# Optimization experiments

Hardware: AMD Instinct MI355X
Metric: run time of the kernel (lower is better)

## Reference

```python
import jax, jax.numpy as jnp
import numpy as np

N = 65536
E = 1048576
DIN = 64
DOUT = 64


def setup_inputs() -> dict:
    key = jax.random.key(0)
    ks = jax.random.split(key, 16)
    inp = {
        'feat': jax.random.normal(ks[0], (N, DIN), dtype=jnp.float32),
        'norm': jax.random.uniform(ks[1], (N, 1), dtype=jnp.float32),
        'src': jax.random.randint(ks[2], (E,), 0, N, dtype=jnp.int32),
        'dst': jax.random.randint(ks[3], (E,), 0, N, dtype=jnp.int32),
    }
    s = 0.05
    inp['W_self'] = jax.random.normal(ks[4], (DOUT, DIN)) * s
    inp['b_self'] = jnp.zeros((DOUT,), jnp.float32)
    inp['W_self_high'] = jax.random.normal(ks[5], (DOUT, DIN)) * s
    inp['b_self_high'] = jnp.zeros((DOUT,), jnp.float32)
    inp['W_neigh'] = jax.random.normal(ks[6], (DOUT, DIN)) * s
    inp['b_neigh'] = jnp.zeros((DOUT,), jnp.float32)
    inp['W_neigh_high'] = jax.random.normal(ks[7], (DOUT, DIN)) * s
    inp['b_neigh_high'] = jnp.zeros((DOUT,), jnp.float32)
    inp['W_id'] = jax.random.normal(ks[8], (DOUT, DIN)) * s
    inp['b_id'] = jnp.zeros((DOUT,), jnp.float32)
    inp['w_att_low'] = jax.random.normal(ks[9], (1, DOUT)) * s
    inp['w_att_high'] = jax.random.normal(ks[10], (1, DOUT)) * s
    inp['w_att_mlp'] = jax.random.normal(ks[11], (1, DOUT)) * s
    inp['W_att'] = jax.random.normal(ks[12], (3, 3)) * s
    return inp


def _linear(x, W, b):
    return x @ W.T + b


def _mean_agg(h, norm, src, dst, n_nodes):
    # copy_src('h','m') of (h * norm), then mean-reduce by dst node
    msg = (h * norm)[src]                                   # [E, D] gather
    summed = jax.ops.segment_sum(msg, dst, num_segments=n_nodes)
    deg = jax.ops.segment_sum(jnp.ones((dst.shape[0],), h.dtype), dst,
                              num_segments=n_nodes)
    return summed / jnp.maximum(deg, 1.0)[:, None]          # zero-in-degree -> 0


def reference(feat, norm, src, dst,
              W_self, b_self, W_self_high, b_self_high,
              W_neigh, b_neigh, W_neigh_high, b_neigh_high,
              W_id, b_id, w_att_low, w_att_high, w_att_mlp, W_att):
    n = feat.shape[0]
    # variant=True branch of acmgraphsage
    self_low = jax.nn.relu(_linear(feat, W_self, b_self))
    self_high = jax.nn.relu(_linear(feat, W_self_high, b_self_high))
    neigh_low = _mean_agg(jax.nn.relu(_linear(feat, W_neigh, b_neigh)),
                          norm, src, dst, n)
    neigh_high = _mean_agg(jax.nn.relu(_linear(feat, W_neigh_high, b_neigh_high)),
                           norm, src, dst, n)
    low = self_low + neigh_low
    high = self_high - neigh_high
    identity = jax.nn.relu(_linear(feat, W_id, b_id))
    # attention: sigmoid of per-branch scalar logits -> 3x3 mix -> softmax/T
    logits = jnp.concatenate([low @ w_att_low.T,
                              high @ w_att_high.T,
                              identity @ w_att_mlp.T], axis=1)   # [N, 3]
    att = jax.nn.softmax((jax.nn.sigmoid(logits) @ W_att.T) / 3.0, axis=1)
    rst = 3.0 * (att[:, 0:1] * low + att[:, 1:2] * high + att[:, 2:3] * identity)
    return rst
```

## Files before the change

### kernel.cpp

```cpp
#include <hip/hip_runtime.h>
#include <stdint.h>


#define NBLK 256
#define NBUC 1024
#define NPB  64
#define GCAP 2048
#define MTOT (NBUC * NBLK)

__device__ __forceinline__ void load_feat(const float* __restrict__ feat, size_t base,
                                          float* __restrict__ f) {
    const float4* fp = (const float4*)(feat + base);
#pragma unroll
    for (int i = 0; i < 16; ++i) {
        float4 v = fp[i];
        f[4 * i + 0] = v.x; f[4 * i + 1] = v.y;
        f[4 * i + 2] = v.z; f[4 * i + 3] = v.w;
    }
}

__device__ __forceinline__ uint32_t bf16_rne(float x) {
    uint32_t u = __float_as_uint(x);
    return (u + 0x7fffu + ((u >> 16) & 1u)) >> 16;
}

__global__ void __launch_bounds__(512)
k_tf_hist(const float* __restrict__ feat, const float* __restrict__ norm,
          const float* __restrict__ Wn, const float* __restrict__ bn,
          const float* __restrict__ Wnh, const float* __restrict__ bnh,
          uint32_t* __restrict__ h_pk,
          const int* __restrict__ dst, int* __restrict__ blk_cnt,
          int N, int E, int nTf)
{
    __shared__ int cnt[NBUC];
    int t = threadIdx.x;

    if ((int)blockIdx.x >= nTf) {
        int hb = blockIdx.x - nTf;
        for (int i = t; i < NBUC; i += 512) cnt[i] = 0;
        __syncthreads();
        int epb = (E + NBLK - 1) / NBLK;
        int eb = hb * epb;
        for (int i0 = t * 8; i0 < epb; i0 += 512 * 8) {
            int e = eb + i0;
            if (e + 8 <= E) {
                int4 d0 = *(const int4*)(dst + e);
                int4 d1 = *(const int4*)(dst + e + 4);
                atomicAdd(&cnt[((unsigned)d0.x) >> 6], 1);
                atomicAdd(&cnt[((unsigned)d0.y) >> 6], 1);
                atomicAdd(&cnt[((unsigned)d0.z) >> 6], 1);
                atomicAdd(&cnt[((unsigned)d0.w) >> 6], 1);
                atomicAdd(&cnt[((unsigned)d1.x) >> 6], 1);
                atomicAdd(&cnt[((unsigned)d1.y) >> 6], 1);
                atomicAdd(&cnt[((unsigned)d1.z) >> 6], 1);
                atomicAdd(&cnt[((unsigned)d1.w) >> 6], 1);
            } else {
                for (int j = 0; j < 8; ++j) {
                    int ee = e + j;
                    if (ee < E) atomicAdd(&cnt[((unsigned)dst[ee]) >> 6], 1);
                }
            }
        }
        __syncthreads();
        for (int i = t; i < NBUC; i += 512)
            blk_cnt[i * NBLK + hb] = cnt[i];
        return;
    }

    int nsub = t & 63;
    int q = __builtin_amdgcn_readfirstlane(t >> 6);
    int n = blockIdx.x * 64 + nsub;
    if (n >= N) return;

    size_t base = (size_t)n << 6;
    float f[64];
    load_feat(feat, base, f);
    float nr = norm[n];

    uint32_t pk[8];
#pragma unroll
    for (int jj = 0; jj < 8; ++jj) {
        int j = q * 8 + jj;
        const float4* rL = (const float4*)(Wn  + ((size_t)j << 6));
        const float4* rH = (const float4*)(Wnh + ((size_t)j << 6));
        float sL = 0.f, sH = 0.f;
#pragma unroll
        for (int k4 = 0; k4 < 16; ++k4) {
            float4 wL = rL[k4];
            float4 wH = rH[k4];
            sL = fmaf(f[4*k4+0], wL.x, sL); sL = fmaf(f[4*k4+1], wL.y, sL);
            sL = fmaf(f[4*k4+2], wL.z, sL); sL = fmaf(f[4*k4+3], wL.w, sL);
            sH = fmaf(f[4*k4+0], wH.x, sH); sH = fmaf(f[4*k4+1], wH.y, sH);
            sH = fmaf(f[4*k4+2], wH.z, sH); sH = fmaf(f[4*k4+3], wH.w, sH);
        }
        float oL = fmaxf(sL + bn[j],  0.f) * nr;
        float oH = fmaxf(sH + bnh[j], 0.f) * nr;
        pk[jj] = bf16_rne(oL) | (bf16_rne(oH) << 16);
    }
    uint4* pp = (uint4*)(h_pk + base + q * 8);
    pp[0] = make_uint4(pk[0], pk[1], pk[2], pk[3]);
    pp[1] = make_uint4(pk[4], pk[5], pk[6], pk[7]);
}

__global__ void __launch_bounds__(256)
k_scan_part(const int* __restrict__ cnt_in, int* __restrict__ part)
{
    __shared__ int red[256];
    int t = threadIdx.x;
    const int4* A4 = (const int4*)cnt_in;
    int4 v = A4[blockIdx.x * 256 + t];
    int s = v.x + v.y + v.z + v.w;
    red[t] = s;
    __syncthreads();
    for (int off = 128; off > 0; off >>= 1) {
        if (t < off) red[t] += red[t + off];
        __syncthreads();
    }
    if (t == 0) part[blockIdx.x] = red[0];
}

__global__ void __launch_bounds__(256)
k_scan_top(const int* __restrict__ part, int* __restrict__ top)
{
    __shared__ int s[256];
    int t = threadIdx.x;
    int mine = part[t];
    s[t] = mine;
    __syncthreads();
    for (int off = 1; off < 256; off <<= 1) {
        int v = s[t];
        int a = (t >= off) ? s[t - off] : 0;
        __syncthreads();
        s[t] = v + a;
        __syncthreads();
    }
    top[t] = s[t] - mine;
}

__global__ void __launch_bounds__(256)
k_scan_down(const int* __restrict__ cnt_in, const int* __restrict__ top,
            int* __restrict__ off_out)
{
    __shared__ int s[256];
    int t = threadIdx.x;
    const int4* A4 = (const int4*)cnt_in;
    int4 v = A4[blockIdx.x * 256 + t];
    int sum = v.x + v.y + v.z + v.w;
    s[t] = sum;
    __syncthreads();
    for (int off = 1; off < 256; off <<= 1) {
        int vv = s[t];
        int a = (t >= off) ? s[t - off] : 0;
        __syncthreads();
        s[t] = vv + a;
        __syncthreads();
    }
    int run = top[blockIdx.x] + s[t] - sum;
    int4 o;
    o.x = run; run += v.x;
    o.y = run; run += v.y;
    o.z = run; run += v.z;
    o.w = run; run += v.w;
    ((int4*)off_out)[blockIdx.x * 256 + t] = o;
    if (blockIdx.x == 255 && t == 255) off_out[MTOT] = run;
}

__global__ void __launch_bounds__(512)
k_bin_scatter(const int* __restrict__ src, const int* __restrict__ dst,
              const int* __restrict__ blk_off, uint32_t* __restrict__ ebuf, int E)
{
    __shared__ int base_[NBUC];
    __shared__ int cnt[NBUC];
    int t = threadIdx.x;
    for (int i = t; i < NBUC; i += 512) {
        base_[i] = blk_off[i * NBLK + blockIdx.x];
        cnt[i] = 0;
    }
    __syncthreads();
    int epb = (E + NBLK - 1) / NBLK;
    int eb = blockIdx.x * epb;
    for (int i0 = t * 8; i0 < epb; i0 += 512 * 8) {
        int e = eb + i0;
        if (e + 8 <= E) {
            int4 d0 = *(const int4*)(dst + e);
            int4 d1 = *(const int4*)(dst + e + 4);
            int4 s0 = *(const int4*)(src + e);
            int4 s1 = *(const int4*)(src + e + 4);
            int da[8] = { d0.x, d0.y, d0.z, d0.w, d1.x, d1.y, d1.z, d1.w };
            int sa[8] = { s0.x, s0.y, s0.z, s0.w, s1.x, s1.y, s1.z, s1.w };
#pragma unroll
            for (int j = 0; j < 8; ++j) {
                int b = ((unsigned)da[j]) >> 6;
                int r = atomicAdd(&cnt[b], 1);
                ebuf[base_[b] + r] = ((uint32_t)(da[j] & 63) << 16) | (uint32_t)sa[j];
            }
        } else {
            for (int j = 0; j < 8; ++j) {
                int ee = e + j;
                if (ee < E) {
                    int d = dst[ee];
                    int b = ((unsigned)d) >> 6;
                    int r = atomicAdd(&cnt[b], 1);
                    ebuf[base_[b] + r] = ((uint32_t)(d & 63) << 16) | (uint32_t)src[ee];
                }
            }
        }
    }
}

__global__ void __launch_bounds__(512)
k_gf(const uint32_t* __restrict__ h_pk, const int* __restrict__ blk_off,
     const uint32_t* __restrict__ ebuf,
     const float* __restrict__ feat,
     const float* __restrict__ Ws, const float* __restrict__ bs,
     const float* __restrict__ Wsh, const float* __restrict__ bsh,
     const float* __restrict__ Wid, const float* __restrict__ bid,
     const float* __restrict__ wl, const float* __restrict__ wh,
     const float* __restrict__ wm, const float* __restrict__ Watt,
     float* __restrict__ out, int N)
{
    __shared__ unsigned short sorted[GCAP];
    __shared__ int s_cnt[NPB];
    __shared__ int s_off[NPB];
    __shared__ uint32_t s_m[NPB][65];
    __shared__ float red[3][8][64];

    int b = blockIdx.x;
    int t = threadIdx.x;
    int es = blk_off[b * NBLK];
    int ee = blk_off[(b + 1) * NBLK];
    int ne = ee - es;
    if (ne > GCAP) ne = GCAP;
    if (t < NPB) s_cnt[t] = 0;
    __syncthreads();

    int ed[4], er[4], esrc[4];
#pragma unroll
    for (int i = 0; i < 4; ++i) {
        int idx = i * 512 + t;
        ed[i] = -1;
        if (idx < ne) {
            uint32_t v = ebuf[es + idx];
            ed[i] = (int)(v >> 16);
            esrc[i] = (int)(v & 0xffffu);
            er[i] = atomicAdd(&s_cnt[ed[i]], 1);
        }
    }
    __syncthreads();
    if (t < 64) {
        int c = s_cnt[t];
        int sc = c;
        for (int o = 1; o < 64; o <<= 1) {
            int u = __shfl_up(sc, o, 64);
            if (t >= o) sc += u;
        }
        s_off[t] = sc - c;
    }
    __syncthreads();
#pragma unroll
    for (int i = 0; i < 4; ++i)
        if (ed[i] >= 0) sorted[s_off[ed[i]] + er[i]] = (unsigned short)esrc[i];
    __syncthreads();

    int w = t >> 6, lane = t & 63;
    for (int dd = 0; dd < 8; ++dd) {
        int d = w * 8 + dd;
        int cd = s_cnt[d];
        int od = s_off[d];
        float accL = 0.f, accH = 0.f;
        int i = 0;
        for (; i + 8 <= cd; i += 8) {
            int s0 = sorted[od + i + 0];
            int s1 = sorted[od + i + 1];
            int s2 = sorted[od + i + 2];
            int s3 = sorted[od + i + 3];
            int s4 = sorted[od + i + 4];
            int s5 = sorted[od + i + 5];
            int s6 = sorted[od + i + 6];
            int s7 = sorted[od + i + 7];
            uint32_t v0 = h_pk[((size_t)s0 << 6) + lane];
            uint32_t v1 = h_pk[((size_t)s1 << 6) + lane];
            uint32_t v2 = h_pk[((size_t)s2 << 6) + lane];
            uint32_t v3 = h_pk[((size_t)s3 << 6) + lane];
            uint32_t v4 = h_pk[((size_t)s4 << 6) + lane];
            uint32_t v5 = h_pk[((size_t)s5 << 6) + lane];
            uint32_t v6 = h_pk[((size_t)s6 << 6) + lane];
            uint32_t v7 = h_pk[((size_t)s7 << 6) + lane];
            accL += (__uint_as_float(v0 << 16) + __uint_as_float(v1 << 16))
                  + (__uint_as_float(v2 << 16) + __uint_as_float(v3 << 16))
                  + (__uint_as_float(v4 << 16) + __uint_as_float(v5 << 16))
                  + (__uint_as_float(v6 << 16) + __uint_as_float(v7 << 16));
            accH += (__uint_as_float(v0 & 0xffff0000u) + __uint_as_float(v1 & 0xffff0000u))
                  + (__uint_as_float(v2 & 0xffff0000u) + __uint_as_float(v3 & 0xffff0000u))
                  + (__uint_as_float(v4 & 0xffff0000u) + __uint_as_float(v5 & 0xffff0000u))
                  + (__uint_as_float(v6 & 0xffff0000u) + __uint_as_float(v7 & 0xffff0000u));
        }
        for (; i + 4 <= cd; i += 4) {
            int s0 = sorted[od + i + 0];
            int s1 = sorted[od + i + 1];
            int s2 = sorted[od + i + 2];
            int s3 = sorted[od + i + 3];
            uint32_t v0 = h_pk[((size_t)s0 << 6) + lane];
            uint32_t v1 = h_pk[((size_t)s1 << 6) + lane];
            uint32_t v2 = h_pk[((size_t)s2 << 6) + lane];
            uint32_t v3 = h_pk[((size_t)s3 << 6) + lane];
            accL += (__uint_as_float(v0 << 16) + __uint_as_float(v1 << 16))
                  + (__uint_as_float(v2 << 16) + __uint_as_float(v3 << 16));
            accH += (__uint_as_float(v0 & 0xffff0000u) + __uint_as_float(v1 & 0xffff0000u))
                  + (__uint_as_float(v2 & 0xffff0000u) + __uint_as_float(v3 & 0xffff0000u));
        }
        for (; i < cd; ++i) {
            int s0 = sorted[od + i];
            uint32_t v0 = h_pk[((size_t)s0 << 6) + lane];
            accL += __uint_as_float(v0 << 16);
            accH += __uint_as_float(v0 & 0xffff0000u);
        }
        float inv = 1.f / fmaxf((float)cd, 1.f);
        s_m[d][lane] = bf16_rne(accL * inv) | (bf16_rne(accH * inv) << 16);
    }
    __syncthreads();

    int nsub = t & 63;
    int q = __builtin_amdgcn_readfirstlane(t >> 6);
    int n = b * 64 + nsub;
    size_t base = (size_t)n << 6;

    float f[64];
    load_feat(feat, base, f);

    float aL[8], aH[8], aI[8];
    float dLp = 0.f, dHp = 0.f, dIp = 0.f;
#pragma unroll
    for (int jj = 0; jj < 8; ++jj) {
        int j = q * 8 + jj;
        const float4* rL = (const float4*)(Ws  + ((size_t)j << 6));
        const float4* rH = (const float4*)(Wsh + ((size_t)j << 6));
        const float4* rI = (const float4*)(Wid + ((size_t)j << 6));
        float sL = 0.f, sH = 0.f, sI = 0.f;
#pragma unroll
        for (int k4 = 0; k4 < 16; ++k4) {
            float4 wL = rL[k4];
            float4 wH = rH[k4];
            float4 wI = rI[k4];
            sL = fmaf(f[4*k4+0], wL.x, sL); sL = fmaf(f[4*k4+1], wL.y, sL);
            sL = fmaf(f[4*k4+2], wL.z, sL); sL = fmaf(f[4*k4+3], wL.w, sL);
            sH = fmaf(f[4*k4+0], wH.x, sH); sH = fmaf(f[4*k4+1], wH.y, sH);
            sH = fmaf(f[4*k4+2], wH.z, sH); sH = fmaf(f[4*k4+3], wH.w, sH);
            sI = fmaf(f[4*k4+0], wI.x, sI); sI = fmaf(f[4*k4+1], wI.y, sI);
            sI = fmaf(f[4*k4+2], wI.z, sI); sI = fmaf(f[4*k4+3], wI.w, sI);
        }
        uint32_t mv = s_m[nsub][j];
        float lowj  = fmaxf(sL + bs[j],  0.f) + __uint_as_float(mv << 16);
        float highj = fmaxf(sH + bsh[j], 0.f) - __uint_as_float(mv & 0xffff0000u);
        float idj   = fmaxf(sI + bid[j], 0.f);
        aL[jj] = lowj; aH[jj] = highj; aI[jj] = idj;
        dLp = fmaf(lowj,  wl[j], dLp);
        dHp = fmaf(highj, wh[j], dHp);
        dIp = fmaf(idj,   wm[j], dIp);
    }

    red[0][q][nsub] = dLp;
    red[1][q][nsub] = dHp;
    red[2][q][nsub] = dIp;
    __syncthreads();
    float dL = 0.f, dH = 0.f, dI = 0.f;
#pragma unroll
    for (int p = 0; p < 8; ++p) {
        dL += red[0][p][nsub];
        dH += red[1][p][nsub];
        dI += red[2][p][nsub];
    }

    float s0 = 1.f / (1.f + expf(-dL));
    float s1 = 1.f / (1.f + expf(-dH));
    float s2 = 1.f / (1.f + expf(-dI));
    const float third = (1.f / 3.f);
    float z0 = (Watt[0] * s0 + Watt[1] * s1 + Watt[2] * s2) * third;
    float z1 = (Watt[3] * s0 + Watt[4] * s1 + Watt[5] * s2) * third;
    float z2 = (Watt[6] * s0 + Watt[7] * s1 + Watt[8] * s2) * third;
    float m = fmaxf(z0, fmaxf(z1, z2));
    float e0 = expf(z0 - m), e1 = expf(z1 - m), e2 = expf(z2 - m);
    float r = 3.f / (e0 + e1 + e2);
    float a0 = e0 * r, a1 = e1 * r, a2 = e2 * r;

    float o[8];
#pragma unroll
    for (int jj = 0; jj < 8; ++jj)
        o[jj] = a0 * aL[jj] + a1 * aH[jj] + a2 * aI[jj];
    float* po = out + base + q * 8;
    *(float4*)(po + 0) = make_float4(o[0], o[1], o[2], o[3]);
    *(float4*)(po + 4) = make_float4(o[4], o[5], o[6], o[7]);
}

extern "C" void kernel_launch(void* const* d_in, const int* in_sizes, int n_in,
                              void* d_out, int out_size, void* d_ws, size_t ws_size,
                              hipStream_t stream) {
    const float* feat         = (const float*)d_in[0];
    const float* norm         = (const float*)d_in[1];
    const int*   src          = (const int*)d_in[2];
    const int*   dst          = (const int*)d_in[3];
    const float* W_self       = (const float*)d_in[4];
    const float* b_self       = (const float*)d_in[5];
    const float* W_self_high  = (const float*)d_in[6];
    const float* b_self_high  = (const float*)d_in[7];
    const float* W_neigh      = (const float*)d_in[8];
    const float* b_neigh      = (const float*)d_in[9];
    const float* W_neigh_high = (const float*)d_in[10];
    const float* b_neigh_high = (const float*)d_in[11];
    const float* W_id         = (const float*)d_in[12];
    const float* b_id         = (const float*)d_in[13];
    const float* w_att_low    = (const float*)d_in[14];
    const float* w_att_high   = (const float*)d_in[15];
    const float* w_att_mlp    = (const float*)d_in[16];
    const float* W_att        = (const float*)d_in[17];

    int N = in_sizes[0] / 64;
    int E = in_sizes[2];
    float* out = (float*)d_out;

    size_t N64 = (size_t)N * 64;

    uint32_t* h_pk    = (uint32_t*)d_ws;
    int*      blk_cnt = (int*)(h_pk + N64);
    int*      blk_off = blk_cnt + MTOT;
    int*      part    = blk_off + MTOT + 16;
    int*      top     = part + 256 + 16;
    uint32_t* ebuf    = (uint32_t*)(top + 256 + 16);

    int nTf = (N + 63) / 64;

    k_tf_hist<<<dim3(nTf + NBLK), dim3(512), 0, stream>>>(
        feat, norm, W_neigh, b_neigh, W_neigh_high, b_neigh_high, h_pk,
        dst, blk_cnt, N, E, nTf);
    k_scan_part<<<dim3(256), dim3(256), 0, stream>>>(blk_cnt, part);
    k_scan_top<<<dim3(1), dim3(256), 0, stream>>>(part, top);
    k_scan_down<<<dim3(256), dim3(256), 0, stream>>>(blk_cnt, top, blk_off);
    k_bin_scatter<<<dim3(NBLK), dim3(512), 0, stream>>>(src, dst, blk_off, ebuf, E);
    k_gf<<<dim3(NBUC), dim3(512), 0, stream>>>(h_pk, blk_off, ebuf, feat,
                                               W_self, b_self,
                                               W_self_high, b_self_high,
                                               W_id, b_id, w_att_low, w_att_high,
                                               w_att_mlp, W_att, out, N);
}
```

Baseline: 139.3 us.

## Stage feature tile in LDS and overlap self-linear compute with neighbor gathers

Loads the block's 64x64 feature tile into shared memory cooperatively and computes the three self/identity linear outputs inside the per-destination loop, right after issuing the first eight neighbor gathers. The aim is to hide gather latency behind FMA work and to drop the 64-float per-thread register feature array. The sorted-index buffer is unioned with the reduction scratch to limit LDS growth, and the 4-wide tail loop is removed. This adds roughly 17KB of LDS, which can lower occupancy. Each lane now reads a row of the padded tile from LDS.

```diff
diff --git a/kernel.cpp b/kernel.cpp
--- a/kernel.cpp
+++ b/kernel.cpp
@@ -7,6 +7,7 @@
 #define NPB  64
 #define GCAP 2048
 #define MTOT (NBUC * NBLK)
+#define NPART 256
 
 __device__ __forceinline__ void load_feat(const float* __restrict__ feat, size_t base,
                                           float* __restrict__ f) {
@@ -122,12 +123,12 @@
 __global__ void __launch_bounds__(256)
 k_scan_top(const int* __restrict__ part, int* __restrict__ top)
 {
-    __shared__ int s[256];
+    __shared__ int s[NPART];
     int t = threadIdx.x;
     int mine = part[t];
     s[t] = mine;
     __syncthreads();
-    for (int off = 1; off < 256; off <<= 1) {
+    for (int off = 1; off < NPART; off <<= 1) {
         int v = s[t];
         int a = (t >= off) ? s[t - off] : 0;
         __syncthreads();
@@ -162,7 +163,7 @@
     o.z = run; run += v.z;
     o.w = run; run += v.w;
     ((int4*)off_out)[blockIdx.x * 256 + t] = o;
-    if (blockIdx.x == 255 && t == 255) off_out[MTOT] = run;
+    if (blockIdx.x == (NPART - 1) && t == 255) off_out[MTOT] = run;
 }
 
 __global__ void __launch_bounds__(512)
@@ -219,14 +220,26 @@
      const float* __restrict__ wm, const float* __restrict__ Watt,
      float* __restrict__ out, int N)
 {
-    __shared__ unsigned short sorted[GCAP];
+    __shared__ union {
+        unsigned short sorted[GCAP + 16];
+        float red[3][8][64];
+    } u;
     __shared__ int s_cnt[NPB];
     __shared__ int s_off[NPB];
     __shared__ uint32_t s_m[NPB][65];
-    __shared__ float red[3][8][64];
+    __shared__ float sf[64][65];
 
     int b = blockIdx.x;
     int t = threadIdx.x;
+
+    {
+        int nn = t >> 3;
+        int c0 = (t & 7) * 8;
+        const float* fp = feat + (((size_t)(b * 64 + nn)) << 6) + c0;
+#pragma unroll
+        for (int k = 0; k < 8; ++k) sf[nn][c0 + k] = fp[k];
+    }
+
     int es = blk_off[b * NBLK];
     int ee = blk_off[(b + 1) * NBLK];
     int ne = ee - es;
@@ -251,33 +264,81 @@
         int c = s_cnt[t];
         int sc = c;
         for (int o = 1; o < 64; o <<= 1) {
-            int u = __shfl_up(sc, o, 64);
-            if (t >= o) sc += u;
+            int uu = __shfl_up(sc, o, 64);
+            if (t >= o) sc += uu;
         }
         s_off[t] = sc - c;
     }
     __syncthreads();
 #pragma unroll
     for (int i = 0; i < 4; ++i)
-        if (ed[i] >= 0) sorted[s_off[ed[i]] + er[i]] = (unsigned short)esrc[i];
-    __syncthreads();
-
-    int w = t >> 6, lane = t & 63;
+        if (ed[i] >= 0) u.sorted[s_off[ed[i]] + er[i]] = (unsigned short)esrc[i];
+    __syncthreads();
+
+    int w = __builtin_amdgcn_readfirstlane(t >> 6);
+    int lane = t & 63;
+    float aL[8], aH[8], aI[8];
+
+#pragma unroll
     for (int dd = 0; dd < 8; ++dd) {
         int d = w * 8 + dd;
         int cd = s_cnt[d];
         int od = s_off[d];
+
+        uint32_t v[8];
+        int n0 = cd < 8 ? cd : 8;
+#pragma unroll
+        for (int k = 0; k < 8; ++k) {
+            int idx = (k < n0) ? (od + k) : od;
+            int s0 = u.sorted[idx];
+            v[k] = (k < n0) ? h_pk[((size_t)s0 << 6) + lane] : 0u;
+        }
+
+        {
+            int j = w * 8 + dd;
+            const float4* rL = (const float4*)(Ws  + ((size_t)j << 6));
+            const float4* rH = (const float4*)(Wsh + ((size_t)j << 6));
+            const float4* rI = (const float4*)(Wid + ((size_t)j << 6));
+            float sL = 0.f, sH = 0.f, sI = 0.f;
+#pragma unroll
+            for (int k4 = 0; k4 < 16; ++k4) {
+                float4 wL = rL[k4];
+                float4 wH = rH[k4];
+                float4 wI = rI[k4];
+                float f0 = sf[lane][4*k4+0];
+                float f1 = sf[lane][4*k4+1];
+                float f2 = sf[lane][4*k4+2];
+                float f3 = sf[lane][4*k4+3];
+                sL = fmaf(f0, wL.x, sL); sL = fmaf(f1, wL.y, sL);
+                sL = fmaf(f2, wL.z, sL); sL = fmaf(f3, wL.w, sL);
+                sH = fmaf(f0, wH.x, sH); sH = fmaf(f1, wH.y, sH);
+                sH = fmaf(f2, wH.z, sH); sH = fmaf(f3, wH.w, sH);
+                sI = fmaf(f0, wI.x, sI); sI = fmaf(f1, wI.y, sI);
+                sI = fmaf(f2, wI.z, sI); sI = fmaf(f3, wI.w, sI);
+            }
+            aL[dd] = fmaxf(sL + bs[j],  0.f);
+            aH[dd] = fmaxf(sH + bsh[j], 0.f);
+            aI[dd] = fmaxf(sI + bid[j], 0.f);
+        }
+
         float accL = 0.f, accH = 0.f;
-        int i = 0;
+#pragma unroll
+        for (int k = 0; k < 8; ++k) {
+            if (k < n0) {
+                accL += __uint_as_float(v[k] << 16);
+                accH += __uint_as_float(v[k] & 0xffff0000u);
+            }
+        }
+        int i = 8;
         for (; i + 8 <= cd; i += 8) {
-            int s0 = sorted[od + i + 0];
-            int s1 = sorted[od + i + 1];
-            int s2 = sorted[od + i + 2];
-            int s3 = sorted[od + i + 3];
-            int s4 = sorted[od + i + 4];
-            int s5 = sorted[od + i + 5];
-            int s6 = sorted[od + i + 6];
-            int s7 = sorted[od + i + 7];
+            int s0 = u.sorted[od + i + 0];
+            int s1 = u.sorted[od + i + 1];
+            int s2 = u.sorted[od + i + 2];
+            int s3 = u.sorted[od + i + 3];
+            int s4 = u.sorted[od + i + 4];
+            int s5 = u.sorted[od + i + 5];
+            int s6 = u.sorted[od + i + 6];
+            int s7 = u.sorted[od + i + 7];
             uint32_t v0 = h_pk[((size_t)s0 << 6) + lane];
             uint32_t v1 = h_pk[((size_t)s1 << 6) + lane];
             uint32_t v2 = h_pk[((size_t)s2 << 6) + lane];
@@ -295,22 +356,8 @@
                   + (__uint_as_float(v4 & 0xffff0000u) + __uint_as_float(v5 & 0xffff0000u))
                   + (__uint_as_float(v6 & 0xffff0000u) + __uint_as_float(v7 & 0xffff0000u));
         }
-        for (; i + 4 <= cd; i += 4) {
-            int s0 = sorted[od + i + 0];
-            int s1 = sorted[od + i + 1];
-            int s2 = sorted[od + i + 2];
-            int s3 = sorted[od + i + 3];
-            uint32_t v0 = h_pk[((size_t)s0 << 6) + lane];
-            uint32_t v1 = h_pk[((size_t)s1 << 6) + lane];
-            uint32_t v2 = h_pk[((size_t)s2 << 6) + lane];
-            uint32_t v3 = h_pk[((size_t)s3 << 6) + lane];
-            accL += (__uint_as_float(v0 << 16) + __uint_as_float(v1 << 16))
-                  + (__uint_as_float(v2 << 16) + __uint_as_float(v3 << 16));
-            accH += (__uint_as_float(v0 & 0xffff0000u) + __uint_as_float(v1 & 0xffff0000u))
-                  + (__uint_as_float(v2 & 0xffff0000u) + __uint_as_float(v3 & 0xffff0000u));
-        }
         for (; i < cd; ++i) {
-            int s0 = sorted[od + i];
+            int s0 = u.sorted[od + i];
             uint32_t v0 = h_pk[((size_t)s0 << 6) + lane];
             accL += __uint_as_float(v0 << 16);
             accH += __uint_as_float(v0 & 0xffff0000u);
@@ -320,55 +367,35 @@
     }
     __syncthreads();
 
-    int nsub = t & 63;
-    int q = __builtin_amdgcn_readfirstlane(t >> 6);
+    int nsub = lane;
+    int q = w;
     int n = b * 64 + nsub;
     size_t base = (size_t)n << 6;
 
-    float f[64];
-    load_feat(feat, base, f);
-
-    float aL[8], aH[8], aI[8];
     float dLp = 0.f, dHp = 0.f, dIp = 0.f;
 #pragma unroll
     for (int jj = 0; jj < 8; ++jj) {
         int j = q * 8 + jj;
-        const float4* rL = (const float4*)(Ws  + ((size_t)j << 6));
-        const float4* rH = (const float4*)(Wsh + ((size_t)j << 6));
-        const float4* rI = (const float4*)(Wid + ((size_t)j << 6));
-        float sL = 0.f, sH = 0.f, sI = 0.f;
-#pragma unroll
-        for (int k4 = 0; k4 < 16; ++k4) {
-            float4 wL = rL[k4];
-            float4 wH = rH[k4];
-            float4 wI = rI[k4];
-            sL = fmaf(f[4*k4+0], wL.x, sL); sL = fmaf(f[4*k4+1], wL.y, sL);
-            sL = fmaf(f[4*k4+2], wL.z, sL); sL = fmaf(f[4*k4+3], wL.w, sL);
-            sH = fmaf(f[4*k4+0], wH.x, sH); sH = fmaf(f[4*k4+1], wH.y, sH);
-            sH = fmaf(f[4*k4+2], wH.z, sH); sH = fmaf(f[4*k4+3], wH.w, sH);
-            sI = fmaf(f[4*k4+0], wI.x, sI); sI = fmaf(f[4*k4+1], wI.y, sI);
-            sI = fmaf(f[4*k4+2], wI.z, sI); sI = fmaf(f[4*k4+3], wI.w, sI);
-        }
         uint32_t mv = s_m[nsub][j];
-        float lowj  = fmaxf(sL + bs[j],  0.f) + __uint_as_float(mv << 16);
-        float highj = fmaxf(sH + bsh[j], 0.f) - __uint_as_float(mv & 0xffff0000u);
-        float idj   = fmaxf(sI + bid[j], 0.f);
-        aL[jj] = lowj; aH[jj] = highj; aI[jj] = idj;
-        dLp = fmaf(lowj,  wl[j], dLp);
-        dHp = fmaf(highj, wh[j], dHp);
-        dIp = fmaf(idj,   wm[j], dIp);
-    }
-
-    red[0][q][nsub] = dLp;
-    red[1][q][nsub] = dHp;
-    red[2][q][nsub] = dIp;
+        float lowj  = aL[jj] + __uint_as_float(mv << 16);
+        float highj = aH[jj] - __uint_as_float(mv & 0xffff0000u);
+        aL[jj] = lowj;
+        aH[jj] = highj;
+        dLp = fmaf(lowj,   wl[j], dLp);
+        dHp = fmaf(highj,  wh[j], dHp);
+        dIp = fmaf(aI[jj], wm[j], dIp);
+    }
+
+    u.red[0][q][nsub] = dLp;
+    u.red[1][q][nsub] = dHp;
+    u.red[2][q][nsub] = dIp;
     __syncthreads();
     float dL = 0.f, dH = 0.f, dI = 0.f;
 #pragma unroll
     for (int p = 0; p < 8; ++p) {
-        dL += red[0][p][nsub];
-        dH += red[1][p][nsub];
-        dI += red[2][p][nsub];
+        dL += u.red[0][p][nsub];
+        dH += u.red[1][p][nsub];
+        dI += u.red[2][p][nsub];
     }
 
     float s0 = 1.f / (1.f + expf(-dL));
@@ -424,17 +451,17 @@
     int*      blk_cnt = (int*)(h_pk + N64);
     int*      blk_off = blk_cnt + MTOT;
     int*      part    = blk_off + MTOT + 16;
-    int*      top     = part + 256 + 16;
-    uint32_t* ebuf    = (uint32_t*)(top + 256 + 16);
+    int*      top     = part + NPART + 16;
+    uint32_t* ebuf    = (uint32_t*)(top + NPART + 16);
 
     int nTf = (N + 63) / 64;
 
     k_tf_hist<<<dim3(nTf + NBLK), dim3(512), 0, stream>>>(
         feat, norm, W_neigh, b_neigh, W_neigh_high, b_neigh_high, h_pk,
         dst, blk_cnt, N, E, nTf);
-    k_scan_part<<<dim3(256), dim3(256), 0, stream>>>(blk_cnt, part);
-    k_scan_top<<<dim3(1), dim3(256), 0, stream>>>(part, top);
-    k_scan_down<<<dim3(256), dim3(256), 0, stream>>>(blk_cnt, top, blk_off);
+    k_scan_part<<<dim3(NPART), dim3(256), 0, stream>>>(blk_cnt, part);
+    k_scan_top<<<dim3(1), dim3(NPART), 0, stream>>>(part, top);
+    k_scan_down<<<dim3(NPART), dim3(256), 0, stream>>>(blk_cnt, top, blk_off);
     k_bin_scatter<<<dim3(NBLK), dim3(512), 0, stream>>>(src, dst, blk_off, ebuf, E);
     k_gf<<<dim3(NBUC), dim3(512), 0, stream>>>(h_pk, blk_off, ebuf, feat,
                                                W_self, b_self,
```

Result: slower. 435.1 us (+212.3%).
